# Kernel optimization log

Measured on AMD Instinct MI355X. Metric: run time of the kernel, lower is better.

## Reference

```python
import jax, jax.numpy as jnp
import numpy as np

DIM = 128
HEADS = 4
DIM_HEAD = 32
NUM_MEM = 4
H = 256
W = 256
SCALE = DIM_HEAD ** -0.5
NORM_SCALE = DIM ** 0.5


def rms_norm(x, gamma):
    # x: (c, h, w); L2-normalize over channel axis, per spatial location
    x32 = x.astype(jnp.float32)
    n = jnp.linalg.norm(x32, ord=2, axis=0)  # (h, w)
    return (x32 / n * (gamma + 1.0) * NORM_SCALE).astype(x.dtype)


def setup_inputs() -> dict:
    key = jax.random.key(0)
    k0, k1, k2, k3 = jax.random.split(key, 4)
    x = jax.random.normal(k0, (DIM, H, W), dtype=jnp.float32)
    gamma1 = jnp.zeros((DIM, 1, 1), dtype=jnp.float32)
    w_qkv = jax.random.normal(k1, (3 * HEADS * DIM_HEAD, DIM), dtype=jnp.float32) * 0.05
    mem_kv = jax.random.normal(k2, (2, HEADS, DIM_HEAD, NUM_MEM), dtype=jnp.float32)
    w_out = jax.random.normal(k3, (DIM, HEADS * DIM_HEAD), dtype=jnp.float32) * 0.05
    b_out = jnp.zeros((DIM,), dtype=jnp.float32)
    gamma2 = jnp.zeros((DIM, 1, 1), dtype=jnp.float32)
    return {"x": x, "gamma1": gamma1, "w_qkv": w_qkv, "mem_kv": mem_kv,
            "w_out": w_out, "b_out": b_out, "gamma2": gamma2}


def reference(x, gamma1, w_qkv, mem_kv, w_out, b_out, gamma2):
    n = H * W
    xn = rms_norm(x, gamma1)
    # 1x1 conv == channel matmul: (3*hid, c) @ (c, h*w)
    qkv = jnp.einsum('oc,cn->on', w_qkv, xn.reshape(DIM, n))
    q, k, v = jnp.split(qkv, 3, axis=0)
    # (h*d, n) -> (h, d, n)
    q = q.reshape(HEADS, DIM_HEAD, n)
    k = k.reshape(HEADS, DIM_HEAD, n)
    v = v.reshape(HEADS, DIM_HEAD, n)
    mk, mv = mem_kv[0], mem_kv[1]  # (h, d, num_mem)
    k = jnp.concatenate([mk, k], axis=-1)  # (h, d, num_mem + n)
    v = jnp.concatenate([mv, v], axis=-1)
    # softmax over feature dim for q (global max subtract), token dim for k
    q = jax.nn.softmax((q - jnp.max(q)).astype(jnp.float32), axis=-2).astype(q.dtype)
    k = jax.nn.softmax((k - jnp.max(k)).astype(jnp.float32), axis=-1).astype(k.dtype)
    q = q * SCALE
    context = jnp.einsum('hdn,hen->hde', k, v)      # (h, d, d)
    out = jnp.einsum('hde,hdn->hen', context, q)    # (h, d, n)
    out = out.reshape(HEADS * DIM_HEAD, H, W)
    out = jnp.einsum('oc,chw->ohw', w_out, out) + b_out[:, None, None]
    return rms_norm(out, gamma2)
```

## Files before the change

kernel.cpp:

```cpp
#include <hip/hip_runtime.h>
#include <hip/hip_bf16.h>
#include <cstddef>


typedef __attribute__((ext_vector_type(8))) short short8;
typedef __attribute__((ext_vector_type(4))) float f32x4;

static constexpr int   NTOK = 65536;
static constexpr float NORM_SCALE_F = 11.313708498984761f;
static constexpr float SCALE_F      = 0.17677669529663687f;

__device__ __forceinline__ unsigned short f2bf(float f) {
  __hip_bfloat16 h = __float2bfloat16(f);
  return *reinterpret_cast<unsigned short*>(&h);
}
__device__ __forceinline__ short sbf(float f) { return (short)f2bf(f); }

__global__ __launch_bounds__(256) void k0_pack(const float* __restrict__ w_qkv,
                                               const float* __restrict__ gamma1,
                                               unsigned short* __restrict__ Wp) {
  const int id = blockIdx.x * 256 + threadIdx.x;
  const int m = id / 16384, p = id % 16384;
  const int j = p & 7, ln = (p >> 3) & 63, frag = p >> 9;
  const int ks = frag & 3, rt = frag >> 2;
  const int row = rt * 16 + (ln & 15);
  const int c = ks * 32 + (ln >> 4) * 8 + j;
  const float v = w_qkv[(m * 128 + row) * 128 + c] * (gamma1[c] + 1.0f) * NORM_SCALE_F;
  Wp[id] = f2bf(v);
}

__global__ __launch_bounds__(512) void k1_kv(const float* __restrict__ x,
                                             const unsigned short* __restrict__ Wkp,
                                             const unsigned short* __restrict__ Wvp,
                                             float* __restrict__ CpAll) {
  __shared__ float cred[4224];
  const int tid = threadIdx.x, wv = tid >> 6, ln = tid & 63;
  const int g4 = ln >> 4, t16 = ln & 15;
  const int n0 = (blockIdx.x * 8 + wv) * 32;

  for (int i = tid; i < 4224; i += 512) cred[i] = 0.f;
  __syncthreads();

  short8 xf[2][4];
  #pragma unroll
  for (int tg = 0; tg < 2; ++tg) {
    float tmp[4][8];
    float sq = 0.f;
    #pragma unroll
    for (int ks = 0; ks < 4; ++ks)
      #pragma unroll
      for (int j = 0; j < 8; ++j) {
        const float f = x[(size_t)(ks * 32 + g4 * 8 + j) * NTOK + n0 + tg * 16 + t16];
        tmp[ks][j] = f;
        sq += f * f;
      }
    sq += __shfl_xor(sq, 16, 64);
    sq += __shfl_xor(sq, 32, 64);
    const float s = rsqrtf(sq);
    #pragma unroll
    for (int ks = 0; ks < 4; ++ks) {
      short8 v;
      #pragma unroll
      for (int j = 0; j < 8; ++j) v[j] = sbf(tmp[ks][j] * s);
      xf[tg][ks] = v;
    }
  }

  #pragma unroll
  for (int h = 0; h < 4; ++h) {
    f32x4 ka[2][2] = {};
    #pragma unroll
    for (int ks = 0; ks < 4; ++ks) {
      const short8 b0 = *reinterpret_cast<const short8*>(Wkp + (((2 * h + 0) * 4 + ks) * 64 + ln) * 8);
      const short8 b1 = *reinterpret_cast<const short8*>(Wkp + (((2 * h + 1) * 4 + ks) * 64 + ln) * 8);
      #pragma unroll
      for (int tg = 0; tg < 2; ++tg) {
        ka[0][tg] = __builtin_amdgcn_mfma_f32_16x16x32_bf16(xf[tg][ks], b0, ka[0][tg], 0, 0, 0);
        ka[1][tg] = __builtin_amdgcn_mfma_f32_16x16x32_bf16(xf[tg][ks], b1, ka[1][tg], 0, 0, 0);
      }
    }
    short8 keA[2];
    #pragma unroll
    for (int mt = 0; mt < 2; ++mt) {
      float sl = 0.f;
      short8 u;
      #pragma unroll
      for (int tg = 0; tg < 2; ++tg)
        #pragma unroll
        for (int r = 0; r < 4; ++r) {
          const float e = __expf(ka[mt][tg][r]);
          sl += e;
          u[tg * 4 + r] = sbf(e);
        }
      keA[mt] = u;
      sl += __shfl_xor(sl, 16, 64);
      sl += __shfl_xor(sl, 32, 64);
      if (g4 == 0) atomicAdd(&cred[4096 + h * 32 + mt * 16 + t16], sl);
    }
    f32x4 va[2][2] = {};
    #pragma unroll
    for (int ks = 0; ks < 4; ++ks) {
      const short8 b0 = *reinterpret_cast<const short8*>(Wvp + (((2 * h + 0) * 4 + ks) * 64 + ln) * 8);
      const short8 b1 = *reinterpret_cast<const short8*>(Wvp + (((2 * h + 1) * 4 + ks) * 64 + ln) * 8);
      #pragma unroll
      for (int tg = 0; tg < 2; ++tg) {
        va[0][tg] = __builtin_amdgcn_mfma_f32_16x16x32_bf16(xf[tg][ks], b0, va[0][tg], 0, 0, 0);
        va[1][tg] = __builtin_amdgcn_mfma_f32_16x16x32_bf16(xf[tg][ks], b1, va[1][tg], 0, 0, 0);
      }
    }
    short8 vB[2];
    #pragma unroll
    for (int et = 0; et < 2; ++et) {
      short8 u;
      #pragma unroll
      for (int tg = 0; tg < 2; ++tg)
        #pragma unroll
        for (int r = 0; r < 4; ++r)
          u[tg * 4 + r] = sbf(va[et][tg][r]);
      vB[et] = u;
    }
    #pragma unroll
    for (int dt = 0; dt < 2; ++dt)
      #pragma unroll
      for (int et = 0; et < 2; ++et) {
        f32x4 zc = {0.f, 0.f, 0.f, 0.f};
        zc = __builtin_amdgcn_mfma_f32_16x16x32_bf16(keA[dt], vB[et], zc, 0, 0, 0);
        #pragma unroll
        for (int r = 0; r < 4; ++r)
          atomicAdd(&cred[h * 1024 + (dt * 16 + g4 * 4 + r) * 32 + et * 16 + t16], zc[r]);
      }
  }

  __syncthreads();
  for (int i = tid; i < 4224; i += 512)
    CpAll[(size_t)blockIdx.x * 4224 + i] = cred[i];
}

__global__ __launch_bounds__(256) void k3a_reduce(const float* __restrict__ CpAll,
                                                  float* __restrict__ Cpp) {
  __shared__ float red[256];
  const int t = threadIdx.x;
  const int eg = blockIdx.x;
  const int ch = blockIdx.y;
  const int e = eg * 128 + (t & 127);
  const int half = t >> 7;
  float s = 0.f;
  for (int bb = 0; bb < 16; ++bb) {
    const int b = ch * 32 + half * 16 + bb;
    s += CpAll[(size_t)b * 4224 + e];
  }
  red[t] = s;
  __syncthreads();
  if (t < 128) Cpp[ch * 4224 + eg * 128 + t] = red[t] + red[t + 128];
}

__global__ __launch_bounds__(256) void k3b1_ctx(const float* __restrict__ Cpp,
                                                const float* __restrict__ mem_kv,
                                                float* __restrict__ ctx) {
  __shared__ float allv[4224];
  const int t = threadIdx.x;
  for (int e = t; e < 4224; e += 256) {
    float s = 0.f;
    #pragma unroll
    for (int c = 0; c < 8; ++c) s += Cpp[c * 4224 + e];
    allv[e] = s;
  }
  __syncthreads();
  for (int e = t; e < 4224; e += 256) {
    if (e < 4096) {
      const int hh = e >> 10, d = (e >> 5) & 31, ev = e & 31;
      float add = 0.f;
      #pragma unroll
      for (int m = 0; m < 4; ++m)
        add += __expf(mem_kv[(hh * 32 + d) * 4 + m]) * mem_kv[512 + (hh * 32 + ev) * 4 + m];
      allv[e] += add;
    } else {
      const int si = e - 4096;
      const int hh = si >> 5, d = si & 31;
      float add = 0.f;
      #pragma unroll
      for (int m = 0; m < 4; ++m) add += __expf(mem_kv[(hh * 32 + d) * 4 + m]);
      allv[e] += add;
    }
  }
  __syncthreads();
  for (int e = t; e < 4096; e += 256)
    ctx[e] = allv[e] / allv[4096 + (e >> 5)];
}

__global__ __launch_bounds__(256) void k3b2_w2(const float* __restrict__ ctx,
                                               const float* __restrict__ w_out,
                                               unsigned short* __restrict__ W2p) {
  const int base = (blockIdx.x * 256 + threadIdx.x) * 8;
  const int ln = (base >> 3) & 63;
  const int frag = base >> 9;
  const int h = frag & 3, ot = frag >> 2;
  const int o = ot * 16 + (ln & 15);
  float wrow[32];
  #pragma unroll
  for (int e = 0; e < 32; ++e) wrow[e] = w_out[o * 128 + h * 32 + e];
  short8 out8;
  #pragma unroll
  for (int j = 0; j < 8; ++j) {
    const int d = (j >> 2) * 16 + ((ln >> 4) << 2) + (j & 3);
    float s = 0.f;
    #pragma unroll
    for (int e = 0; e < 32; ++e)
      s += wrow[e] * ctx[h * 1024 + d * 32 + e];
    out8[j] = sbf(s * SCALE_F);
  }
  *reinterpret_cast<short8*>(W2p + base) = out8;
}

__global__ __launch_bounds__(256) void k5_out(const float* __restrict__ x,
                                              const unsigned short* __restrict__ Wqp,
                                              const unsigned short* __restrict__ W2p,
                                              const float* __restrict__ b_out,
                                              const float* __restrict__ gamma2,
                                              float* __restrict__ y) {
  const int tid = threadIdx.x, wv = tid >> 6, ln = tid & 63;
  const int g4 = ln >> 4, t16 = ln & 15;
  const int n0 = (blockIdx.x * 4 + wv) * 32;

  short8 xf[2][4];
  #pragma unroll
  for (int tg = 0; tg < 2; ++tg) {
    float tmp[4][8];
    float sq = 0.f;
    #pragma unroll
    for (int ks = 0; ks < 4; ++ks)
      #pragma unroll
      for (int j = 0; j < 8; ++j) {
        const float f = x[(size_t)(ks * 32 + g4 * 8 + j) * NTOK + n0 + tg * 16 + t16];
        tmp[ks][j] = f;
        sq += f * f;
      }
    sq += __shfl_xor(sq, 16, 64);
    sq += __shfl_xor(sq, 32, 64);
    const float s = rsqrtf(sq);
    #pragma unroll
    for (int ks = 0; ks < 4; ++ks) {
      short8 v;
      #pragma unroll
      for (int j = 0; j < 8; ++j) v[j] = sbf(tmp[ks][j] * s);
      xf[tg][ks] = v;
    }
  }

  short8 qB[4][2];
  #pragma unroll
  for (int h = 0; h < 4; ++h) {
    f32x4 qa[2][2] = {};
    #pragma unroll
    for (int ks = 0; ks < 4; ++ks) {
      const short8 a0 = *reinterpret_cast<const short8*>(Wqp + (((2 * h + 0) * 4 + ks) * 64 + ln) * 8);
      const short8 a1 = *reinterpret_cast<const short8*>(Wqp + (((2 * h + 1) * 4 + ks) * 64 + ln) * 8);
      #pragma unroll
      for (int tg = 0; tg < 2; ++tg) {
        qa[0][tg] = __builtin_amdgcn_mfma_f32_16x16x32_bf16(a0, xf[tg][ks], qa[0][tg], 0, 0, 0);
        qa[1][tg] = __builtin_amdgcn_mfma_f32_16x16x32_bf16(a1, xf[tg][ks], qa[1][tg], 0, 0, 0);
      }
    }
    #pragma unroll
    for (int tg = 0; tg < 2; ++tg) {
      float ev[2][4];
      float ss = 0.f;
      #pragma unroll
      for (int rtl = 0; rtl < 2; ++rtl)
        #pragma unroll
        for (int r = 0; r < 4; ++r) {
          ev[rtl][r] = __expf(qa[rtl][tg][r]);
          ss += ev[rtl][r];
        }
      ss += __shfl_xor(ss, 16, 64);
      ss += __shfl_xor(ss, 32, 64);
      const float inv = 1.0f / ss;
      short8 u;
      #pragma unroll
      for (int rtl = 0; rtl < 2; ++rtl)
        #pragma unroll
        for (int r = 0; r < 4; ++r)
          u[rtl * 4 + r] = sbf(ev[rtl][r] * inv);
      qB[h][tg] = u;
    }
  }

  f32x4 z[8][2] = {};
  #pragma unroll
  for (int h = 0; h < 4; ++h)
    #pragma unroll
    for (int ot = 0; ot < 8; ++ot) {
      const short8 a = *reinterpret_cast<const short8*>(W2p + ((ot * 4 + h) * 64 + ln) * 8);
      #pragma unroll
      for (int tg = 0; tg < 2; ++tg)
        z[ot][tg] = __builtin_amdgcn_mfma_f32_16x16x32_bf16(a, qB[h][tg], z[ot][tg], 0, 0, 0);
    }

  float ssq[2] = {0.f, 0.f};
  #pragma unroll
  for (int ot = 0; ot < 8; ++ot) {
    const float4 bb = *reinterpret_cast<const float4*>(b_out + ot * 16 + g4 * 4);
    const float barr[4] = {bb.x, bb.y, bb.z, bb.w};
    #pragma unroll
    for (int tg = 0; tg < 2; ++tg)
      #pragma unroll
      for (int r = 0; r < 4; ++r) {
        const float zb = z[ot][tg][r] + barr[r];
        z[ot][tg][r] = zb;
        ssq[tg] += zb * zb;
      }
  }
  float rr[2];
  #pragma unroll
  for (int tg = 0; tg < 2; ++tg) {
    float s = ssq[tg];
    s += __shfl_xor(s, 16, 64);
    s += __shfl_xor(s, 32, 64);
    rr[tg] = rsqrtf(s);
  }
  #pragma unroll
  for (int ot = 0; ot < 8; ++ot) {
    const float4 gg = *reinterpret_cast<const float4*>(gamma2 + ot * 16 + g4 * 4);
    const float garr[4] = {gg.x, gg.y, gg.z, gg.w};
    #pragma unroll
    for (int tg = 0; tg < 2; ++tg)
      #pragma unroll
      for (int r = 0; r < 4; ++r) {
        const int row = ot * 16 + g4 * 4 + r;
        y[(size_t)row * NTOK + n0 + tg * 16 + t16] =
            z[ot][tg][r] * rr[tg] * (garr[r] + 1.0f) * NORM_SCALE_F;
      }
  }
}

extern "C" void kernel_launch(void* const* d_in, const int* in_sizes, int n_in,
                              void* d_out, int out_size, void* d_ws, size_t ws_size,
                              hipStream_t stream) {
  const float* x      = (const float*)d_in[0];
  const float* gamma1 = (const float*)d_in[1];
  const float* w_qkv  = (const float*)d_in[2];
  const float* mem_kv = (const float*)d_in[3];
  const float* w_out  = (const float*)d_in[4];
  const float* b_out  = (const float*)d_in[5];
  const float* gamma2 = (const float*)d_in[6];
  float* out = (float*)d_out;
  float* ws  = (float*)d_ws;

  unsigned short* Wqp = (unsigned short*)ws;
  unsigned short* Wkp = Wqp + 16384;
  unsigned short* Wvp = Wkp + 16384;
  unsigned short* W2p = Wvp + 16384;
  float* CpAll = ws + 32768;
  float* Cpp   = CpAll + 1081344;
  float* ctx   = Cpp + 33792;

  hipLaunchKernelGGL(k0_pack,    dim3(192),    dim3(256), 0, stream, w_qkv, gamma1, Wqp);
  hipLaunchKernelGGL(k1_kv,      dim3(256),    dim3(512), 0, stream, x, Wkp, Wvp, CpAll);
  hipLaunchKernelGGL(k3a_reduce, dim3(33, 8),  dim3(256), 0, stream, CpAll, Cpp);
  hipLaunchKernelGGL(k3b1_ctx,   dim3(1),      dim3(256), 0, stream, Cpp, mem_kv, ctx);
  hipLaunchKernelGGL(k3b2_w2,    dim3(8),      dim3(256), 0, stream, ctx, w_out, W2p);
  hipLaunchKernelGGL(k5_out,     dim3(512),    dim3(256), 0, stream, x, Wqp, W2p, b_out, gamma2, out);
}
```

Baseline: 173.5 us.

## Precompute normalized bf16 token-major input once and share across kernels

```diff
diff --git a/kernel.cpp b/kernel.cpp
--- a/kernel.cpp
+++ b/kernel.cpp
@@ -29,7 +29,31 @@
   Wp[id] = f2bf(v);
 }
 
-__global__ __launch_bounds__(512) void k1_kv(const float* __restrict__ x,
+__global__ __launch_bounds__(256) void k_norm(const float* __restrict__ x,
+                                              unsigned short* __restrict__ xn) {
+  const int t = threadIdx.x;
+  const int tok = blockIdx.x * 64 + (t >> 2);
+  const int cg = (t & 3) * 32;
+  float v[32];
+  float sq = 0.f;
+  #pragma unroll
+  for (int j = 0; j < 32; ++j) {
+    v[j] = x[(size_t)(cg + j) * NTOK + tok];
+    sq += v[j] * v[j];
+  }
+  sq += __shfl_xor(sq, 1, 64);
+  sq += __shfl_xor(sq, 2, 64);
+  const float s = rsqrtf(sq);
+  #pragma unroll
+  for (int g = 0; g < 4; ++g) {
+    short8 o;
+    #pragma unroll
+    for (int j = 0; j < 8; ++j) o[j] = sbf(v[g * 8 + j] * s);
+    *reinterpret_cast<short8*>(xn + (size_t)tok * 128 + cg + g * 8) = o;
+  }
+}
+
+__global__ __launch_bounds__(512) void k1_kv(const unsigned short* __restrict__ xn,
                                              const unsigned short* __restrict__ Wkp,
                                              const unsigned short* __restrict__ Wvp,
                                              float* __restrict__ CpAll) {
@@ -43,28 +67,11 @@
 
   short8 xf[2][4];
   #pragma unroll
-  for (int tg = 0; tg < 2; ++tg) {
-    float tmp[4][8];
-    float sq = 0.f;
+  for (int tg = 0; tg < 2; ++tg)
     #pragma unroll
     for (int ks = 0; ks < 4; ++ks)
-      #pragma unroll
-      for (int j = 0; j < 8; ++j) {
-        const float f = x[(size_t)(ks * 32 + g4 * 8 + j) * NTOK + n0 + tg * 16 + t16];
-        tmp[ks][j] = f;
-        sq += f * f;
-      }
-    sq += __shfl_xor(sq, 16, 64);
-    sq += __shfl_xor(sq, 32, 64);
-    const float s = rsqrtf(sq);
-    #pragma unroll
-    for (int ks = 0; ks < 4; ++ks) {
-      short8 v;
-      #pragma unroll
-      for (int j = 0; j < 8; ++j) v[j] = sbf(tmp[ks][j] * s);
-      xf[tg][ks] = v;
-    }
-  }
+      xf[tg][ks] = *reinterpret_cast<const short8*>(
+          xn + (size_t)(n0 + tg * 16 + t16) * 128 + ks * 32 + g4 * 8);
 
   #pragma unroll
   for (int h = 0; h < 4; ++h) {
@@ -212,7 +219,7 @@
   *reinterpret_cast<short8*>(W2p + base) = out8;
 }
 
-__global__ __launch_bounds__(256) void k5_out(const float* __restrict__ x,
+__global__ __launch_bounds__(256) void k5_out(const unsigned short* __restrict__ xn,
                                               const unsigned short* __restrict__ Wqp,
                                               const unsigned short* __restrict__ W2p,
                                               const float* __restrict__ b_out,
@@ -224,28 +231,11 @@
 
   short8 xf[2][4];
   #pragma unroll
-  for (int tg = 0; tg < 2; ++tg) {
-    float tmp[4][8];
-    float sq = 0.f;
+  for (int tg = 0; tg < 2; ++tg)
     #pragma unroll
     for (int ks = 0; ks < 4; ++ks)
-      #pragma unroll
-      for (int j = 0; j < 8; ++j) {
-        const float f = x[(size_t)(ks * 32 + g4 * 8 + j) * NTOK + n0 + tg * 16 + t16];
-        tmp[ks][j] = f;
-        sq += f * f;
-      }
-    sq += __shfl_xor(sq, 16, 64);
-    sq += __shfl_xor(sq, 32, 64);
-    const float s = rsqrtf(sq);
-    #pragma unroll
-    for (int ks = 0; ks < 4; ++ks) {
-      short8 v;
-      #pragma unroll
-      for (int j = 0; j < 8; ++j) v[j] = sbf(tmp[ks][j] * s);
-      xf[tg][ks] = v;
-    }
-  }
+      xf[tg][ks] = *reinterpret_cast<const short8*>(
+          xn + (size_t)(n0 + tg * 16 + t16) * 128 + ks * 32 + g4 * 8);
 
   short8 qB[4][2];
   #pragma unroll
@@ -353,11 +343,13 @@
   float* CpAll = ws + 32768;
   float* Cpp   = CpAll + 1081344;
   float* ctx   = Cpp + 33792;
+  unsigned short* xn = (unsigned short*)(ws + 1152000);
 
   hipLaunchKernelGGL(k0_pack,    dim3(192),    dim3(256), 0, stream, w_qkv, gamma1, Wqp);
-  hipLaunchKernelGGL(k1_kv,      dim3(256),    dim3(512), 0, stream, x, Wkp, Wvp, CpAll);
+  hipLaunchKernelGGL(k_norm,     dim3(1024),   dim3(256), 0, stream, x, xn);
+  hipLaunchKernelGGL(k1_kv,      dim3(256),    dim3(512), 0, stream, xn, Wkp, Wvp, CpAll);
   hipLaunchKernelGGL(k3a_reduce, dim3(33, 8),  dim3(256), 0, stream, CpAll, Cpp);
   hipLaunchKernelGGL(k3b1_ctx,   dim3(1),      dim3(256), 0, stream, Cpp, mem_kv, ctx);
   hipLaunchKernelGGL(k3b2_w2,    dim3(8),      dim3(256), 0, stream, ctx, w_out, W2p);
-  hipLaunchKernelGGL(k5_out,     dim3(512),    dim3(256), 0, stream, x, Wqp, W2p, b_out, gamma2, out);
-}
+  hipLaunchKernelGGL(k5_out,     dim3(512),    dim3(256), 0, stream, xn, Wqp, W2p, b_out, gamma2, out);
+}
```

New measurement: 182.3 us. +5.1%, slower.
